# Optimization experiments

Measured on AMD Instinct MI355X. Metric: run time of the kernel, lower is better.

The kernel has to match this reference:

```python
import jax, jax.numpy as jnp
import numpy as np

E, D, H = 16, 768, 768  # experts, d_model, d_hidden (FMoETransformerMLP(16, 768, 768))
B, N = 32, 197


def setup_inputs() -> dict:
    key = jax.random.key(0)
    ks = jax.random.split(key, 7)
    s = 0.02
    return {
        "x": jax.random.normal(ks[0], (B, N, D), dtype=jnp.float32),
        "W1": jax.random.normal(ks[1], (E, H, D), dtype=jnp.float32) * s,
        "b1": jax.random.normal(ks[2], (E, H), dtype=jnp.float32) * s,
        "W2": jax.random.normal(ks[3], (E, D, H), dtype=jnp.float32) * s,
        "b2": jax.random.normal(ks[4], (E, D), dtype=jnp.float32) * s,
        "Wg": jax.random.normal(ks[5], (E, D), dtype=jnp.float32) * s,
        "bg": jnp.zeros((E,), dtype=jnp.float32),
    }


def reference(x, W1, b1, W2, b2, Wg, bg):
    # FMoETransformerMLP forward: flatten tokens, gate, dispatch, expert MLP, combine.
    Bx, Nx, Dx = x.shape
    t = x.reshape(-1, Dx)                     # [T, D] tokens
    logits = t @ Wg.T + bg                    # [T, E] gate logits
    idx = jnp.argmax(logits, axis=-1)
    out = jnp.zeros_like(t)
    for e in range(W1.shape[0]):              # small fixed expert loop
        mask = (idx == e).astype(t.dtype)[:, None]
        h = jax.nn.gelu(t @ W1[e].T + b1[e], approximate=False)  # htoh4 + GELU
        y = h @ W2[e].T + b2[e]                                   # h4toh
        out = out + mask * y
    return out.reshape(Bx, Nx, Dx)
```

## Files before the change

kernel.cpp:

```cpp
#include <hip/hip_runtime.h>
#include <hip/hip_bf16.h>
#include <math.h>
#include <type_traits>

#define T_TOK 6304
#define DMODEL 768
#define NEXP 16
#define NGATE 394

typedef __bf16 bf16x8 __attribute__((ext_vector_type(8)));
typedef float f32x4 __attribute__((ext_vector_type(4)));

__device__ __forceinline__ unsigned short f2bf(float f) {
    __hip_bfloat16 b = __float2bfloat16(f);
    return __builtin_bit_cast(unsigned short, b);
}
__device__ __forceinline__ unsigned int pack2(float lo, float hi) {
    return (unsigned int)f2bf(lo) | ((unsigned int)f2bf(hi) << 16);
}

__global__ __launch_bounds__(256) void gate_kernel(
    const float* __restrict__ x, const float* __restrict__ Wg,
    const float* __restrict__ bg, int* __restrict__ cnt, int* __restrict__ list,
    unsigned short* __restrict__ xb)
{
    __shared__ __align__(16) float wlds[16][772];
    __shared__ double lg[16][17];
    const int tid = threadIdx.x;
    {
        const float4* src = (const float4*)Wg;
#pragma unroll
        for (int v = tid, it = 0; it < 12; ++it, v += 256) {
            float4 wv = src[v];
            int row = v / 192, col = (v - row * 192) * 4;
            *(float4*)&wlds[row][col] = wv;
        }
    }
    __syncthreads();

    const int tt = tid >> 4;
    const int e  = tid & 15;
    const int t  = blockIdx.x * 16 + tt;
    const float4* xr = (const float4*)(x + (size_t)t * DMODEL);
    double s0 = 0, s1 = 0, s2 = 0, s3 = 0;
#pragma unroll 8
    for (int i = 0; i < DMODEL / 4; ++i) {
        float4 a = xr[i];
        float4 w = *(const float4*)&wlds[e][i * 4];
        s0 += (double)a.x * (double)w.x;
        s1 += (double)a.y * (double)w.y;
        s2 += (double)a.z * (double)w.z;
        s3 += (double)a.w * (double)w.w;
    }
    lg[tt][e] = (s0 + s1) + (s2 + s3);
    if (xb) {
        uint4* dst = (uint4*)(xb + (size_t)t * DMODEL + e * 48);
#pragma unroll
        for (int u = 0; u < 6; ++u) {
            float4 a = xr[e * 12 + 2 * u], b = xr[e * 12 + 2 * u + 1];
            dst[u] = make_uint4(pack2(a.x, a.y), pack2(a.z, a.w),
                                pack2(b.x, b.y), pack2(b.z, b.w));
        }
    }
    __syncthreads();
    if (e == 0) {
        double best = -1e300; int bi = 0;
#pragma unroll
        for (int k = 0; k < NEXP; ++k) {
            double v = lg[tt][k] + (double)bg[k];
            if (v > best) { best = v; bi = k; }
        }
        int pos = atomicAdd(&cnt[bi], 1);
        list[bi * T_TOK + pos] = t;
    }
}

template<int GELU, int PACKED_IN, int PACKED_OUT, typename TW, typename TOUT>
__global__ __launch_bounds__(256, 4) void expert_gemm(
    const unsigned short* __restrict__ in, const TW* __restrict__ Wb,
    const float* __restrict__ bias, const int* __restrict__ cnt,
    const int* __restrict__ list, TOUT* __restrict__ outp)
{
    constexpr int BK = 64, LDK = 72;
    constexpr bool W_F32 = std::is_same<TW, float>::value;
    __shared__ __align__(16) unsigned short At[2][64][LDK];
    __shared__ __align__(16) unsigned short Bt[2][64][LDK];
    __shared__ int toks[64];

    const int bx = blockIdx.x;
    const int g  = bx >> 3;
    const int e  = (bx & 7) + 8 * (g / 12);
    const int nb = g % 12;
    const int c = cnt[e];
    int off = 0;
    if (PACKED_IN || PACKED_OUT)
        for (int k = 0; k < e; ++k) off += cnt[k];
    const int n0 = nb * 64;
    const int tid = threadIdx.x, lane = tid & 63, w = tid >> 6;
    const int rg = w & 1, cgp = w >> 1;
    const int l15 = lane & 15, q8 = (lane >> 4) * 8, q = lane >> 4;
    const int sr = tid >> 2, sk = (tid & 3) * 16;

    const TW* bsrc = Wb + (size_t)e * DMODEL * DMODEL + (size_t)(n0 + sr) * DMODEL + sk;
    const int* lst = list + e * T_TOK;

    uint4 pa[2], pb[2];
    float4 fb[4];

    for (int yt = blockIdx.y; yt * 64 < c; yt += 8) {
        const int m0 = yt * 64;
        __syncthreads();
        if (!PACKED_OUT && tid < 64) {
            int mi = m0 + tid;
            toks[tid] = lst[mi < c ? mi : c - 1];
        }
        const int ma0 = m0 + sr;
        const int mac = ma0 < c ? ma0 : c - 1;
        const unsigned short* asrc = PACKED_IN
            ? in + (size_t)(off + mac) * DMODEL + sk
            : in + (size_t)lst[mac] * DMODEL + sk;

        f32x4 acc[2][2];
#pragma unroll
        for (int i = 0; i < 2; ++i)
#pragma unroll
            for (int j = 0; j < 2; ++j) acc[i][j] = (f32x4){0.f, 0.f, 0.f, 0.f};

        auto load_regs = [&](int k0) {
            const uint4* s = (const uint4*)(asrc + k0);
            pa[0] = s[0]; pa[1] = s[1];
            if constexpr (W_F32) {
                const float4* t2 = (const float4*)(bsrc + k0);
                fb[0] = t2[0]; fb[1] = t2[1]; fb[2] = t2[2]; fb[3] = t2[3];
            } else {
                const uint4* t2 = (const uint4*)(bsrc + k0);
                pb[0] = t2[0]; pb[1] = t2[1];
            }
        };
        auto store_tiles = [&](int buf) {
            *(uint4*)&At[buf][sr][sk] = pa[0]; *(uint4*)&At[buf][sr][sk + 8] = pa[1];
            if constexpr (W_F32) {
                uint4 w0, w1;
                w0.x = pack2(fb[0].x, fb[0].y); w0.y = pack2(fb[0].z, fb[0].w);
                w0.z = pack2(fb[1].x, fb[1].y); w0.w = pack2(fb[1].z, fb[1].w);
                w1.x = pack2(fb[2].x, fb[2].y); w1.y = pack2(fb[2].z, fb[2].w);
                w1.z = pack2(fb[3].x, fb[3].y); w1.w = pack2(fb[3].z, fb[3].w);
                *(uint4*)&Bt[buf][sr][sk] = w0; *(uint4*)&Bt[buf][sr][sk + 8] = w1;
            } else {
                *(uint4*)&Bt[buf][sr][sk] = pb[0]; *(uint4*)&Bt[buf][sr][sk + 8] = pb[1];
            }
        };

        load_regs(0);
        store_tiles(0);
#pragma unroll 1
        for (int it = 0; it < DMODEL / BK; ++it) {
            __syncthreads();
            if (it + 1 < DMODEL / BK) load_regs((it + 1) * BK);
            const int buf = it & 1;
#pragma unroll
            for (int kk = 0; kk < BK; kk += 32) {
                bf16x8 a0 = *(const bf16x8*)&At[buf][rg * 32 + l15][kk + q8];
                bf16x8 a1 = *(const bf16x8*)&At[buf][rg * 32 + 16 + l15][kk + q8];
                bf16x8 b0 = *(const bf16x8*)&Bt[buf][cgp * 32 + l15][kk + q8];
                bf16x8 b1 = *(const bf16x8*)&Bt[buf][cgp * 32 + 16 + l15][kk + q8];
                acc[0][0] = __builtin_amdgcn_mfma_f32_16x16x32_bf16(b0, a0, acc[0][0], 0, 0, 0);
                acc[0][1] = __builtin_amdgcn_mfma_f32_16x16x32_bf16(b1, a0, acc[0][1], 0, 0, 0);
                acc[1][0] = __builtin_amdgcn_mfma_f32_16x16x32_bf16(b0, a1, acc[1][0], 0, 0, 0);
                acc[1][1] = __builtin_amdgcn_mfma_f32_16x16x32_bf16(b1, a1, acc[1][1], 0, 0, 0);
            }
            if (it + 1 < DMODEL / BK) store_tiles(buf ^ 1);
        }

        __syncthreads();
        float (*C)[68] = reinterpret_cast<float (*)[68]>(&At[0][0][0]);
#pragma unroll
        for (int i = 0; i < 2; ++i) {
            const int mrow = rg * 32 + i * 16 + l15;
#pragma unroll
            for (int j = 0; j < 2; ++j) {
                const int lc = cgp * 32 + j * 16 + q * 4;
                const float4 bv = *(const float4*)&bias[e * DMODEL + n0 + lc];
                float v0 = acc[i][j][0] + bv.x;
                float v1 = acc[i][j][1] + bv.y;
                float v2 = acc[i][j][2] + bv.z;
                float v3 = acc[i][j][3] + bv.w;
                if (GELU) {
                    v0 = 0.5f * v0 * (1.f + erff(v0 * 0.70710678118654752f));
                    v1 = 0.5f * v1 * (1.f + erff(v1 * 0.70710678118654752f));
                    v2 = 0.5f * v2 * (1.f + erff(v2 * 0.70710678118654752f));
                    v3 = 0.5f * v3 * (1.f + erff(v3 * 0.70710678118654752f));
                }
                *(float4*)&C[mrow][lc] = make_float4(v0, v1, v2, v3);
            }
        }
        __syncthreads();
        {
            const int row = tid >> 2, q2 = tid & 3;
            if (m0 + row < c) {
                const size_t rb = PACKED_OUT
                    ? (size_t)(off + m0 + row) * DMODEL
                    : (size_t)toks[row] * DMODEL;
                const int cg0 = q2 * 16;
                const float* cr = &C[row][cg0];
                if constexpr (std::is_same<TOUT, float>::value) {
                    float4* dst = (float4*)&outp[rb + n0 + cg0];
                    dst[0] = *(const float4*)&cr[0];
                    dst[1] = *(const float4*)&cr[4];
                    dst[2] = *(const float4*)&cr[8];
                    dst[3] = *(const float4*)&cr[12];
                } else {
                    uint4* dst = (uint4*)&outp[rb + n0 + cg0];
                    dst[0] = make_uint4(pack2(cr[0], cr[1]),  pack2(cr[2], cr[3]),
                                        pack2(cr[4], cr[5]),  pack2(cr[6], cr[7]));
                    dst[1] = make_uint4(pack2(cr[8], cr[9]),  pack2(cr[10], cr[11]),
                                        pack2(cr[12], cr[13]), pack2(cr[14], cr[15]));
                }
            }
        }
    }
}

template<int GELU, typename TA, typename TW, typename TOUT>
__global__ __launch_bounds__(256, 4) void expert_layer(
    const TA* __restrict__ in, const TW* __restrict__ W,
    const float* __restrict__ bias, const int* __restrict__ cnt,
    const int* __restrict__ list, TOUT* __restrict__ outp)
{
    constexpr int BK = 64, LDK = 72;
    constexpr bool A_F32 = std::is_same<TA, float>::value;
    constexpr bool W_F32 = std::is_same<TW, float>::value;
    __shared__ __align__(16) unsigned short At[2][64][LDK];
    __shared__ __align__(16) unsigned short Bt[2][64][LDK];
    __shared__ int toks[64];

    const int bx = blockIdx.x;
    const int e = bx / 12, nb = bx % 12;
    const int c = cnt[e];
    const int n0 = nb * 64;
    const int tid = threadIdx.x, lane = tid & 63, w = tid >> 6;
    const int rg = w & 1, cgp = w >> 1;
    const int l15 = lane & 15, q8 = (lane >> 4) * 8, q = lane >> 4;
    const int sr = tid >> 2, sk = (tid & 3) * 16;

    const TW* bsrc = W + (size_t)e * DMODEL * DMODEL + (size_t)(n0 + sr) * DMODEL + sk;
    const int* lst = list + e * T_TOK;

    uint4 pa[2], pb[2];
    float4 fa[4], fb[4];

    for (int yt = blockIdx.y; yt * 64 < c; yt += 8) {
        const int m0 = yt * 64;
        __syncthreads();
        if (tid < 64) {
            int mi = m0 + tid;
            toks[tid] = lst[mi < c ? mi : c - 1];
        }
        int ma = m0 + sr;
        const TA* asrc = in + (size_t)lst[ma < c ? ma : c - 1] * DMODEL + sk;

        f32x4 acc[2][2];
#pragma unroll
        for (int i = 0; i < 2; ++i)
#pragma unroll
            for (int j = 0; j < 2; ++j) acc[i][j] = (f32x4){0.f, 0.f, 0.f, 0.f};

        auto load_regs = [&](int k0) {
            if constexpr (A_F32) {
                const float4* s = (const float4*)(asrc + k0);
                fa[0] = s[0]; fa[1] = s[1]; fa[2] = s[2]; fa[3] = s[3];
            } else {
                const uint4* s = (const uint4*)(asrc + k0);
                pa[0] = s[0]; pa[1] = s[1];
            }
            if constexpr (W_F32) {
                const float4* s = (const float4*)(bsrc + k0);
                fb[0] = s[0]; fb[1] = s[1]; fb[2] = s[2]; fb[3] = s[3];
            } else {
                const uint4* s = (const uint4*)(bsrc + k0);
                pb[0] = s[0]; pb[1] = s[1];
            }
        };
        auto store_tiles = [&](int buf) {
            if constexpr (A_F32) {
                uint4 w0, w1;
                w0.x = pack2(fa[0].x, fa[0].y); w0.y = pack2(fa[0].z, fa[0].w);
                w0.z = pack2(fa[1].x, fa[1].y); w0.w = pack2(fa[1].z, fa[1].w);
                w1.x = pack2(fa[2].x, fa[2].y); w1.y = pack2(fa[2].z, fa[2].w);
                w1.z = pack2(fa[3].x, fa[3].y); w1.w = pack2(fa[3].z, fa[3].w);
                *(uint4*)&At[buf][sr][sk] = w0; *(uint4*)&At[buf][sr][sk + 8] = w1;
            } else {
                *(uint4*)&At[buf][sr][sk] = pa[0]; *(uint4*)&At[buf][sr][sk + 8] = pa[1];
            }
            if constexpr (W_F32) {
                uint4 w0, w1;
                w0.x = pack2(fb[0].x, fb[0].y); w0.y = pack2(fb[0].z, fb[0].w);
                w0.z = pack2(fb[1].x, fb[1].y); w0.w = pack2(fb[1].z, fb[1].w);
                w1.x = pack2(fb[2].x, fb[2].y); w1.y = pack2(fb[2].z, fb[2].w);
                w1.z = pack2(fb[3].x, fb[3].y); w1.w = pack2(fb[3].z, fb[3].w);
                *(uint4*)&Bt[buf][sr][sk] = w0; *(uint4*)&Bt[buf][sr][sk + 8] = w1;
            } else {
                *(uint4*)&Bt[buf][sr][sk] = pb[0]; *(uint4*)&Bt[buf][sr][sk + 8] = pb[1];
            }
        };

        load_regs(0);
        store_tiles(0);
#pragma unroll 1
        for (int it = 0; it < DMODEL / BK; ++it) {
            __syncthreads();
            if (it + 1 < DMODEL / BK) load_regs((it + 1) * BK);
            const int buf = it & 1;
#pragma unroll
            for (int kk = 0; kk < BK; kk += 32) {
                bf16x8 a0 = *(const bf16x8*)&At[buf][rg * 32 + l15][kk + q8];
                bf16x8 a1 = *(const bf16x8*)&At[buf][rg * 32 + 16 + l15][kk + q8];
                bf16x8 b0 = *(const bf16x8*)&Bt[buf][cgp * 32 + l15][kk + q8];
                bf16x8 b1 = *(const bf16x8*)&Bt[buf][cgp * 32 + 16 + l15][kk + q8];
                acc[0][0] = __builtin_amdgcn_mfma_f32_16x16x32_bf16(a0, b0, acc[0][0], 0, 0, 0);
                acc[0][1] = __builtin_amdgcn_mfma_f32_16x16x32_bf16(a0, b1, acc[0][1], 0, 0, 0);
                acc[1][0] = __builtin_amdgcn_mfma_f32_16x16x32_bf16(a1, b0, acc[1][0], 0, 0, 0);
                acc[1][1] = __builtin_amdgcn_mfma_f32_16x16x32_bf16(a1, b1, acc[1][1], 0, 0, 0);
            }
            if (it + 1 < DMODEL / BK) store_tiles(buf ^ 1);
        }

#pragma unroll
        for (int i = 0; i < 2; ++i) {
#pragma unroll
            for (int j = 0; j < 2; ++j) {
                int col = n0 + cgp * 32 + j * 16 + l15;
                float bv = bias[e * DMODEL + col];
#pragma unroll
                for (int r = 0; r < 4; ++r) {
                    int mrow = rg * 32 + i * 16 + q * 4 + r;
                    if (m0 + mrow < c) {
                        float val = acc[i][j][r] + bv;
                        if (GELU) val = 0.5f * val * (1.f + erff(val * 0.70710678118654752f));
                        size_t idx = (size_t)toks[mrow] * DMODEL + col;
                        if constexpr (std::is_same<TOUT, float>::value) outp[idx] = val;
                        else outp[idx] = f2bf(val);
                    }
                }
            }
        }
    }
}

extern "C" void kernel_launch(void* const* d_in, const int* in_sizes, int n_in,
                              void* d_out, int out_size, void* d_ws, size_t ws_size,
                              hipStream_t stream)
{
    const float* x  = (const float*)d_in[0];
    const float* W1 = (const float*)d_in[1];
    const float* b1 = (const float*)d_in[2];
    const float* W2 = (const float*)d_in[3];
    const float* b2 = (const float*)d_in[4];
    const float* Wg = (const float*)d_in[5];
    const float* bg = (const float*)d_in[6];
    float* out = (float*)d_out;

    char* ws   = (char*)d_ws;
    int*  cnt  = (int*)ws;
    int*  list = (int*)(ws + 256);
    unsigned short* xb  = (unsigned short*)(ws + 403712);
    unsigned short* h   = (unsigned short*)(ws + 10086656);
    const bool big = ws_size >= (size_t)19769600;

    hipMemsetAsync(cnt, 0, 256, stream);
    dim3 grid(12 * NEXP, 8);
    if (big) {
        gate_kernel<<<dim3(NGATE), dim3(256), 0, stream>>>(
            x, Wg, bg, cnt, list, xb);
        expert_gemm<1, 0, 1, float, unsigned short>
            <<<grid, dim3(256), 0, stream>>>(xb, W1, b1, cnt, list, h);
        expert_gemm<0, 1, 0, float, float>
            <<<grid, dim3(256), 0, stream>>>(h, W2, b2, cnt, list, out);
    } else {
        gate_kernel<<<dim3(NGATE), dim3(256), 0, stream>>>(
            x, Wg, bg, cnt, list, nullptr);
        expert_layer<1, float, float, unsigned short>
            <<<grid, dim3(256), 0, stream>>>(x, W1, b1, cnt, list, h);
        expert_layer<0, unsigned short, float, float>
            <<<grid, dim3(256), 0, stream>>>(h, W2, b2, cnt, list, out);
    }
}
```

Baseline: 284.9 us.

## Enlarge expert GEMM M tile to 128 rows for better weight reuse

The expert GEMM tile grows from 64 to 128 token rows per block. Each warp now computes a 64x32 output sub-tile, so each B fragment feeds four A fragments and each converted fp32 weight tile is reused across twice as many tokens. The grid's y dimension is halved and the launch bounds drop to 2 blocks per SM to make room for the larger shared memory and accumulator footprint. This costs occupancy and may leave more padding waste on experts with few tokens.

```diff
diff --git a/kernel.cpp b/kernel.cpp
--- a/kernel.cpp
+++ b/kernel.cpp
@@ -76,16 +76,17 @@
 }
 
 template<int GELU, int PACKED_IN, int PACKED_OUT, typename TW, typename TOUT>
-__global__ __launch_bounds__(256, 4) void expert_gemm(
+__global__ __launch_bounds__(256, 2) void expert_gemm(
     const unsigned short* __restrict__ in, const TW* __restrict__ Wb,
     const float* __restrict__ bias, const int* __restrict__ cnt,
     const int* __restrict__ list, TOUT* __restrict__ outp)
 {
-    constexpr int BK = 64, LDK = 72;
+    constexpr int BM = 128, BK = 64, LDK = 72;
+    constexpr int NIT = DMODEL / BK;
     constexpr bool W_F32 = std::is_same<TW, float>::value;
-    __shared__ __align__(16) unsigned short At[2][64][LDK];
+    __shared__ __align__(16) unsigned short At[2][BM][LDK];
     __shared__ __align__(16) unsigned short Bt[2][64][LDK];
-    __shared__ int toks[64];
+    __shared__ int toks[BM];
 
     const int bx = blockIdx.x;
     const int g  = bx >> 3;
@@ -97,89 +98,95 @@
         for (int k = 0; k < e; ++k) off += cnt[k];
     const int n0 = nb * 64;
     const int tid = threadIdx.x, lane = tid & 63, w = tid >> 6;
-    const int rg = w & 1, cgp = w >> 1;
+    const int wr = w & 1, wc = w >> 1;
     const int l15 = lane & 15, q8 = (lane >> 4) * 8, q = lane >> 4;
-    const int sr = tid >> 2, sk = (tid & 3) * 16;
-
-    const TW* bsrc = Wb + (size_t)e * DMODEL * DMODEL + (size_t)(n0 + sr) * DMODEL + sk;
+    const int ar = tid >> 1, aseg = (tid & 1) * 32;
+    const int wrow = tid >> 2, wsk = (tid & 3) * 16;
+
+    const TW* bsrc = Wb + (size_t)e * DMODEL * DMODEL + (size_t)(n0 + wrow) * DMODEL + wsk;
     const int* lst = list + e * T_TOK;
 
-    uint4 pa[2], pb[2];
-    float4 fb[4];
-
-    for (int yt = blockIdx.y; yt * 64 < c; yt += 8) {
-        const int m0 = yt * 64;
+    for (int yt = blockIdx.y; yt * BM < c; yt += 4) {
+        const int m0 = yt * BM;
         __syncthreads();
-        if (!PACKED_OUT && tid < 64) {
+        if (!PACKED_OUT && tid < BM) {
             int mi = m0 + tid;
             toks[tid] = lst[mi < c ? mi : c - 1];
         }
-        const int ma0 = m0 + sr;
+        const int ma0 = m0 + ar;
         const int mac = ma0 < c ? ma0 : c - 1;
         const unsigned short* asrc = PACKED_IN
-            ? in + (size_t)(off + mac) * DMODEL + sk
-            : in + (size_t)lst[mac] * DMODEL + sk;
-
-        f32x4 acc[2][2];
-#pragma unroll
-        for (int i = 0; i < 2; ++i)
+            ? in + (size_t)(off + mac) * DMODEL + aseg
+            : in + (size_t)lst[mac] * DMODEL + aseg;
+
+        f32x4 acc[4][2];
+#pragma unroll
+        for (int i = 0; i < 4; ++i)
 #pragma unroll
             for (int j = 0; j < 2; ++j) acc[i][j] = (f32x4){0.f, 0.f, 0.f, 0.f};
+
+        uint4 pa[4];
+        float4 fb[4];
+        uint4 pbq[2];
 
         auto load_regs = [&](int k0) {
             const uint4* s = (const uint4*)(asrc + k0);
-            pa[0] = s[0]; pa[1] = s[1];
+            pa[0] = s[0]; pa[1] = s[1]; pa[2] = s[2]; pa[3] = s[3];
             if constexpr (W_F32) {
                 const float4* t2 = (const float4*)(bsrc + k0);
                 fb[0] = t2[0]; fb[1] = t2[1]; fb[2] = t2[2]; fb[3] = t2[3];
             } else {
                 const uint4* t2 = (const uint4*)(bsrc + k0);
-                pb[0] = t2[0]; pb[1] = t2[1];
+                pbq[0] = t2[0]; pbq[1] = t2[1];
             }
         };
         auto store_tiles = [&](int buf) {
-            *(uint4*)&At[buf][sr][sk] = pa[0]; *(uint4*)&At[buf][sr][sk + 8] = pa[1];
+            *(uint4*)&At[buf][ar][aseg]      = pa[0];
+            *(uint4*)&At[buf][ar][aseg + 8]  = pa[1];
+            *(uint4*)&At[buf][ar][aseg + 16] = pa[2];
+            *(uint4*)&At[buf][ar][aseg + 24] = pa[3];
             if constexpr (W_F32) {
                 uint4 w0, w1;
                 w0.x = pack2(fb[0].x, fb[0].y); w0.y = pack2(fb[0].z, fb[0].w);
                 w0.z = pack2(fb[1].x, fb[1].y); w0.w = pack2(fb[1].z, fb[1].w);
                 w1.x = pack2(fb[2].x, fb[2].y); w1.y = pack2(fb[2].z, fb[2].w);
                 w1.z = pack2(fb[3].x, fb[3].y); w1.w = pack2(fb[3].z, fb[3].w);
-                *(uint4*)&Bt[buf][sr][sk] = w0; *(uint4*)&Bt[buf][sr][sk + 8] = w1;
-            } else {
-                *(uint4*)&Bt[buf][sr][sk] = pb[0]; *(uint4*)&Bt[buf][sr][sk + 8] = pb[1];
+                *(uint4*)&Bt[buf][wrow][wsk] = w0; *(uint4*)&Bt[buf][wrow][wsk + 8] = w1;
+            } else {
+                *(uint4*)&Bt[buf][wrow][wsk] = pbq[0];
+                *(uint4*)&Bt[buf][wrow][wsk + 8] = pbq[1];
             }
         };
 
         load_regs(0);
         store_tiles(0);
 #pragma unroll 1
-        for (int it = 0; it < DMODEL / BK; ++it) {
+        for (int it = 0; it < NIT; ++it) {
             __syncthreads();
-            if (it + 1 < DMODEL / BK) load_regs((it + 1) * BK);
+            if (it + 1 < NIT) load_regs((it + 1) * BK);
             const int buf = it & 1;
 #pragma unroll
             for (int kk = 0; kk < BK; kk += 32) {
-                bf16x8 a0 = *(const bf16x8*)&At[buf][rg * 32 + l15][kk + q8];
-                bf16x8 a1 = *(const bf16x8*)&At[buf][rg * 32 + 16 + l15][kk + q8];
-                bf16x8 b0 = *(const bf16x8*)&Bt[buf][cgp * 32 + l15][kk + q8];
-                bf16x8 b1 = *(const bf16x8*)&Bt[buf][cgp * 32 + 16 + l15][kk + q8];
-                acc[0][0] = __builtin_amdgcn_mfma_f32_16x16x32_bf16(b0, a0, acc[0][0], 0, 0, 0);
-                acc[0][1] = __builtin_amdgcn_mfma_f32_16x16x32_bf16(b1, a0, acc[0][1], 0, 0, 0);
-                acc[1][0] = __builtin_amdgcn_mfma_f32_16x16x32_bf16(b0, a1, acc[1][0], 0, 0, 0);
-                acc[1][1] = __builtin_amdgcn_mfma_f32_16x16x32_bf16(b1, a1, acc[1][1], 0, 0, 0);
-            }
-            if (it + 1 < DMODEL / BK) store_tiles(buf ^ 1);
+                bf16x8 b0 = *(const bf16x8*)&Bt[buf][wc * 32 + l15][kk + q8];
+                bf16x8 b1 = *(const bf16x8*)&Bt[buf][wc * 32 + 16 + l15][kk + q8];
+#pragma unroll
+                for (int i = 0; i < 4; ++i) {
+                    bf16x8 ai = *(const bf16x8*)&At[buf][wr * 64 + i * 16 + l15][kk + q8];
+                    acc[i][0] = __builtin_amdgcn_mfma_f32_16x16x32_bf16(b0, ai, acc[i][0], 0, 0, 0);
+                    acc[i][1] = __builtin_amdgcn_mfma_f32_16x16x32_bf16(b1, ai, acc[i][1], 0, 0, 0);
+                }
+            }
+            if (it + 1 < NIT) store_tiles(buf ^ 1);
         }
 
         __syncthreads();
         float (*C)[68] = reinterpret_cast<float (*)[68]>(&At[0][0][0]);
 #pragma unroll
-        for (int i = 0; i < 2; ++i) {
-            const int mrow = rg * 32 + i * 16 + l15;
+        for (int i = 0; i < 4; ++i) {
+            const int mrow = wr * 64 + i * 16 + l15;
 #pragma unroll
             for (int j = 0; j < 2; ++j) {
-                const int lc = cgp * 32 + j * 16 + q * 4;
+                const int lc = wc * 32 + j * 16 + q * 4;
                 const float4 bv = *(const float4*)&bias[e * DMODEL + n0 + lc];
                 float v0 = acc[i][j][0] + bv.x;
                 float v1 = acc[i][j][1] + bv.y;
@@ -196,25 +203,24 @@
         }
         __syncthreads();
         {
-            const int row = tid >> 2, q2 = tid & 3;
+            const int row = tid >> 1, half = (tid & 1) * 32;
             if (m0 + row < c) {
                 const size_t rb = PACKED_OUT
                     ? (size_t)(off + m0 + row) * DMODEL
                     : (size_t)toks[row] * DMODEL;
-                const int cg0 = q2 * 16;
-                const float* cr = &C[row][cg0];
+                const float* cr = &C[row][half];
                 if constexpr (std::is_same<TOUT, float>::value) {
-                    float4* dst = (float4*)&outp[rb + n0 + cg0];
-                    dst[0] = *(const float4*)&cr[0];
-                    dst[1] = *(const float4*)&cr[4];
-                    dst[2] = *(const float4*)&cr[8];
-                    dst[3] = *(const float4*)&cr[12];
+                    float4* dst = (float4*)&outp[rb + n0 + half];
+#pragma unroll
+                    for (int u = 0; u < 8; ++u) dst[u] = *(const float4*)&cr[4 * u];
                 } else {
-                    uint4* dst = (uint4*)&outp[rb + n0 + cg0];
-                    dst[0] = make_uint4(pack2(cr[0], cr[1]),  pack2(cr[2], cr[3]),
-                                        pack2(cr[4], cr[5]),  pack2(cr[6], cr[7]));
-                    dst[1] = make_uint4(pack2(cr[8], cr[9]),  pack2(cr[10], cr[11]),
-                                        pack2(cr[12], cr[13]), pack2(cr[14], cr[15]));
+                    uint4* dst = (uint4*)&outp[rb + n0 + half];
+#pragma unroll
+                    for (int u = 0; u < 4; ++u)
+                        dst[u] = make_uint4(pack2(cr[8*u+0], cr[8*u+1]),
+                                            pack2(cr[8*u+2], cr[8*u+3]),
+                                            pack2(cr[8*u+4], cr[8*u+5]),
+                                            pack2(cr[8*u+6], cr[8*u+7]));
                 }
             }
         }
@@ -368,10 +374,10 @@
     const bool big = ws_size >= (size_t)19769600;
 
     hipMemsetAsync(cnt, 0, 256, stream);
-    dim3 grid(12 * NEXP, 8);
     if (big) {
         gate_kernel<<<dim3(NGATE), dim3(256), 0, stream>>>(
             x, Wg, bg, cnt, list, xb);
+        dim3 grid(12 * NEXP, 4);
         expert_gemm<1, 0, 1, float, unsigned short>
             <<<grid, dim3(256), 0, stream>>>(xb, W1, b1, cnt, list, h);
         expert_gemm<0, 1, 0, float, float>
@@ -379,6 +385,7 @@
     } else {
         gate_kernel<<<dim3(NGATE), dim3(256), 0, stream>>>(
             x, Wg, bg, cnt, list, nullptr);
+        dim3 grid(12 * NEXP, 8);
         expert_layer<1, float, float, unsigned short>
             <<<grid, dim3(256), 0, stream>>>(x, W1, b1, cnt, list, h);
         expert_layer<0, unsigned short, float, float>
```

New measurement: 268.2 us. -5.9%, faster.
